# Performance work log

Hardware: AMD Instinct MI355X
Metric: run time of the kernel (lower is better)

Reference implementation:

```python
import jax, jax.numpy as jnp
import numpy as np

N = 80000      # num nodes total (8 graphs x 10000 vars)
E = 2560000    # num edges (avg degree 32)
EMB = 64       # embedding_layer_dim
POS = 16       # positional_features_dims
DG = 64        # dim_gnn
IN0 = 2 * EMB + POS          # 144, first conv in
IN1 = DG + 2 * EMB           # 192, second conv in / BN dim
EPS = 1e-5


def _lin_init(key, fan_in, fan_out):
    return jax.random.normal(key, (fan_in, fan_out), jnp.float32) / np.sqrt(fan_in)


def setup_inputs() -> dict:
    key = jax.random.key(0)
    ks = jax.random.split(key, 16)
    inp = {}
    inp["x1"] = jax.random.normal(ks[0], (N, EMB), jnp.float32)
    inp["x2"] = jax.random.normal(ks[1], (N, EMB), jnp.float32)
    inp["random_dims"] = jax.random.normal(ks[2], (N, POS), jnp.float32)
    inp["batch"] = jnp.sort(jax.random.randint(ks[3], (N,), 0, 8)).astype(jnp.int64)
    inp["x_j_mask"] = jnp.ones((E,), jnp.float32)
    inp["edge_index"] = jax.random.randint(ks[4], (2, E), 0, N).astype(jnp.int64)
    # GCNConv weights (PyG: lin then aggregate, bias added after)
    inp["conv0_w"] = _lin_init(ks[5], IN0, DG)
    inp["conv0_b"] = jnp.zeros((DG,), jnp.float32)
    inp["conv1_w"] = _lin_init(ks[6], IN1, DG)
    inp["conv1_b"] = jnp.zeros((DG,), jnp.float32)
    # BatchNorms after each conv (dim = DG + 2*EMB = 192)
    inp["bn0_g"] = jnp.ones((IN1,), jnp.float32)
    inp["bn0_b"] = jnp.zeros((IN1,), jnp.float32)
    inp["bn1_g"] = jnp.ones((IN1,), jnp.float32)
    inp["bn1_b"] = jnp.zeros((IN1,), jnp.float32)
    # MLP head: mlp[:-2] = [192->64, 64->64], mlp[-2] = 64->32 (final ->1 not applied here)
    inp["mlp0_w"] = _lin_init(ks[7], IN1, DG)
    inp["mlp0_b"] = jnp.zeros((DG,), jnp.float32)
    inp["mlp1_w"] = _lin_init(ks[8], DG, DG)
    inp["mlp1_b"] = jnp.zeros((DG,), jnp.float32)
    inp["mlp2_w"] = _lin_init(ks[9], DG, DG // 2)
    inp["mlp2_b"] = jnp.zeros((DG // 2,), jnp.float32)
    inp["bnm0_g"] = jnp.ones((DG,), jnp.float32)
    inp["bnm0_b"] = jnp.zeros((DG,), jnp.float32)
    inp["bnm1_g"] = jnp.ones((DG,), jnp.float32)
    inp["bnm1_b"] = jnp.zeros((DG,), jnp.float32)
    inp["bnm2_g"] = jnp.ones((DG // 2,), jnp.float32)
    inp["bnm2_b"] = jnp.zeros((DG // 2,), jnp.float32)
    return inp


def _batchnorm(x, g, b):
    m = x.mean(axis=0)
    v = jnp.var(x, axis=0)  # biased var, as torch BN uses for normalization
    return (x - m) * jax.lax.rsqrt(v + EPS) * g + b


def _gcn_conv(x, w, b, row, col, coef):
    # coef = deg^-1/2[row] * deg^-1/2[col] * x_j_mask, per edge
    h = x @ w                                   # [N, out]
    msg = coef[:, None] * h[row]                # gather + scale, [E, out]
    agg = jax.ops.segment_sum(msg, col, num_segments=N)
    return agg + b


def reference(x1, x2, random_dims, batch, x_j_mask, edge_index,
              conv0_w, conv0_b, conv1_w, conv1_b,
              bn0_g, bn0_b, bn1_g, bn1_b,
              mlp0_w, mlp0_b, mlp1_w, mlp1_b, mlp2_w, mlp2_b,
              bnm0_g, bnm0_b, bnm1_g, bnm1_b, bnm2_g, bnm2_b):
    row, col = edge_index[0], edge_index[1]
    # gcn_norm with add_self_loops=False, unit edge weights
    deg = jax.ops.segment_sum(jnp.ones((E,), x1.dtype), col, num_segments=N)
    dis = jnp.where(deg > 0, jax.lax.rsqrt(jnp.maximum(deg, 1.0)), 0.0)
    coef = dis[row] * dis[col] * x_j_mask       # edge mutilation mask applied to messages

    x = jnp.concatenate([x1, x2, random_dims], axis=1)  # [N, 144]
    # GNN layer 0
    h = jax.nn.elu(_gcn_conv(x, conv0_w, conv0_b, row, col, coef))
    x = _batchnorm(jnp.concatenate([x1, x2, h], axis=1), bn0_g, bn0_b)
    # GNN layer 1
    h = jax.nn.elu(_gcn_conv(x, conv1_w, conv1_b, row, col, coef))
    x = _batchnorm(jnp.concatenate([x1, x2, h], axis=1), bn1_g, bn1_b)
    # MLP head (from_node_to_out: mlp[:-2] with bns_mlp[:-1], then mlp[-2] with bns_mlp[-1])
    x = _batchnorm(jax.nn.elu(x @ mlp0_w + mlp0_b), bnm0_g, bnm0_b)
    x = _batchnorm(jax.nn.elu(x @ mlp1_w + mlp1_b), bnm1_g, bnm1_b)
    x = _batchnorm(jax.nn.elu(x @ mlp2_w + mlp2_b), bnm2_g, bnm2_b)
    return x  # [N, DG//2]
```

## Files before the change

kernel.cpp:

```cpp
#include <hip/hip_runtime.h>
#include <math.h>

#define NN 80000
#define NE 2560000
#define NBK 313
#define BN_EPS 1e-5f

typedef __attribute__((ext_vector_type(8))) short short8;
typedef __attribute__((ext_vector_type(8))) unsigned short ushort8;
typedef __attribute__((ext_vector_type(4))) float f32x4;

#define OFF_DIS     0
#define OFF_ROWPTR  80000
#define OFF_CURSOR  160004
#define OFF_DEG     240004
#define OFF_PERM    320004
#define OFF_XB      (OFF_PERM + 2*NE)
#define OFF_RDB     (OFF_XB + NN*64)
#define OFF_B1      (OFF_RDB + NN*16)
#define OFF_B2      (OFF_B1 + NN*32)
#define OFF_B3      (OFF_B2 + NN*32)
#define OFF_WP      (OFF_B3 + NN*32)
#define OFF_BV      (OFF_WP + 20480)
#define OFF_STATS   (OFF_BV + 320)

__device__ __forceinline__ ushort f2b(float f) {
    union { float f; unsigned u; } x; x.f = f;
    return (ushort)((x.u + 0x7FFF + ((x.u >> 16) & 1)) >> 16);
}
__device__ __forceinline__ float b2f(ushort u) {
    union { unsigned u; float f; } x; x.u = ((unsigned)u) << 16;
    return x.f;
}

__global__ void k_deg(const int* __restrict__ col, int* __restrict__ deg) {
    int e = blockIdx.x * blockDim.x + threadIdx.x;
    if (e < NE) atomicAdd(&deg[col[e]], 1);
}

__global__ void __launch_bounds__(256) k_scanA(const int* __restrict__ deg,
                                               float* __restrict__ dis,
                                               int* __restrict__ bsum) {
    int i = blockIdx.x * 256 + threadIdx.x;
    int d = i < NN ? deg[i] : 0;
    if (i < NN) dis[i] = d > 0 ? rsqrtf((float)d) : 0.f;
    __shared__ int red[256];
    red[threadIdx.x] = d;
    __syncthreads();
    for (int off = 128; off > 0; off >>= 1) {
        if (threadIdx.x < off) red[threadIdx.x] += red[threadIdx.x + off];
        __syncthreads();
    }
    if (threadIdx.x == 0) bsum[blockIdx.x] = red[0];
}

__global__ void __launch_bounds__(512) k_scanB(const int* __restrict__ bsum,
                                               int* __restrict__ boff,
                                               int* __restrict__ rowptr) {
    __shared__ int s[512];
    int t = threadIdx.x;
    int v = t < NBK ? bsum[t] : 0;
    s[t] = v;
    __syncthreads();
    for (int off = 1; off < 512; off <<= 1) {
        int u = t >= off ? s[t - off] : 0;
        __syncthreads();
        s[t] += u;
        __syncthreads();
    }
    if (t < NBK) boff[t] = s[t] - v;
    if (t == NBK - 1) rowptr[NN] = s[t];
}

__global__ void __launch_bounds__(256) k_scanC(const int* __restrict__ deg,
                                               const int* __restrict__ boff,
                                               int* __restrict__ rowptr) {
    int i = blockIdx.x * 256 + threadIdx.x;
    int d = i < NN ? deg[i] : 0;
    __shared__ int s[256];
    s[threadIdx.x] = d;
    __syncthreads();
    for (int off = 1; off < 256; off <<= 1) {
        int u = threadIdx.x >= off ? s[threadIdx.x - off] : 0;
        __syncthreads();
        s[threadIdx.x] += u;
        __syncthreads();
    }
    if (i < NN) rowptr[i] = boff[blockIdx.x] + s[threadIdx.x] - d;
}

__global__ void __launch_bounds__(256) k_scat1(const int* __restrict__ erow,
                                               const int* __restrict__ ecol,
                                               const float* __restrict__ mask,
                                               const float* __restrict__ dis,
                                               const int* __restrict__ rowptr,
                                               int* __restrict__ bcursor,
                                               int2* __restrict__ pbuf) {
    __shared__ int hist[NBK], base[NBK];
    for (int i = threadIdx.x; i < NBK; i += 256) hist[i] = 0;
    __syncthreads();
    int e0 = blockIdx.x * 4096;
    int r[16], c[16], rk[16];
    float cf[16];
    #pragma unroll
    for (int i = 0; i < 16; i++) {
        int e = e0 + i * 256 + threadIdx.x;
        if (e < NE) {
            r[i] = erow[e]; c[i] = ecol[e];
            cf[i] = dis[r[i]] * dis[c[i]] * mask[e];
            rk[i] = atomicAdd(&hist[c[i] >> 8], 1);
        } else c[i] = -1;
    }
    __syncthreads();
    for (int b = threadIdx.x; b < NBK; b += 256) {
        int h = hist[b];
        base[b] = h ? atomicAdd(&bcursor[b], h) : 0;
    }
    __syncthreads();
    #pragma unroll
    for (int i = 0; i < 16; i++) {
        if (c[i] >= 0) {
            int b = c[i] >> 8;
            int addr = rowptr[b << 8] + base[b] + rk[i];
            pbuf[addr] = make_int2((r[i] << 8) | (c[i] & 255), __float_as_int(cf[i]));
        }
    }
}

__global__ void __launch_bounds__(256) k_scat2(const int* __restrict__ rowptr,
                                               const int2* __restrict__ pbuf,
                                               int2* __restrict__ perm) {
    __shared__ int rbase[257];
    __shared__ int lcur[256];
    int b = blockIdx.x;
    int c0 = b << 8;
    int ncols = (NN - c0) < 256 ? (NN - c0) : 256;
    int s0 = rowptr[c0];
    if (threadIdx.x < ncols) rbase[threadIdx.x] = rowptr[c0 + threadIdx.x] - s0;
    if (threadIdx.x == 0) rbase[ncols] = rowptr[c0 + ncols] - s0;
    lcur[threadIdx.x] = 0;
    __syncthreads();
    int cnt = rbase[ncols];
    for (int i = threadIdx.x; i < cnt; i += 256) {
        int2 rec = pbuf[s0 + i];
        int crel = rec.x & 255;
        int rr = rec.x >> 8;
        int slot = rbase[crel] + atomicAdd(&lcur[crel], 1);
        perm[s0 + slot] = make_int2(rr, rec.y);
    }
}

__global__ void __launch_bounds__(256) k_prepstats(const float* __restrict__ x1,
                                                   const float* __restrict__ x2,
                                                   const float* __restrict__ rd,
                                                   ushort* __restrict__ xb,
                                                   ushort* __restrict__ rdb,
                                                   float* __restrict__ st) {
    int wave = threadIdx.x >> 6, lane = threadIdx.x & 63;
    float s1 = 0, q1 = 0, s2 = 0, q2 = 0;
    for (int n = blockIdx.x * 4 + wave; n < NN; n += gridDim.x * 4) {
        float a = x1[(size_t)n * 64 + lane];
        float b = x2[(size_t)n * 64 + lane];
        s1 += a; q1 += a * a; s2 += b; q2 += b * b;
        xb[(size_t)n * 128 + lane]      = f2b(a);
        xb[(size_t)n * 128 + 64 + lane] = f2b(b);
        if (lane < 32)
            rdb[(size_t)n * 32 + lane] = lane < 16 ? f2b(rd[(size_t)n * 16 + lane]) : 0;
    }
    __shared__ float red[4][256];
    red[0][threadIdx.x] = s1; red[1][threadIdx.x] = q1;
    red[2][threadIdx.x] = s2; red[3][threadIdx.x] = q2;
    __syncthreads();
    if (threadIdx.x < 64) {
        int l = threadIdx.x;
        atomicAdd(&st[l],       red[0][l] + red[0][l+64] + red[0][l+128] + red[0][l+192]);
        atomicAdd(&st[128 + l], red[1][l] + red[1][l+64] + red[1][l+128] + red[1][l+192]);
        atomicAdd(&st[64 + l],  red[2][l] + red[2][l+64] + red[2][l+128] + red[2][l+192]);
        atomicAdd(&st[192 + l], red[3][l] + red[3][l+64] + red[3][l+128] + red[3][l+192]);
    }
}

__global__ void k_foldw0(const float* __restrict__ W, ushort* __restrict__ Wp) {
    for (int idx = threadIdx.x; idx < 160 * 64; idx += 256) {
        int k = idx >> 6, c = idx & 63;
        float val = k < 144 ? W[k * 64 + c] : 0.f;
        int ks = k >> 5, j = k & 7, kg = (k >> 3) & 3;
        int l = kg * 16 + (c & 15), ct = c >> 4;
        Wp[((ks * 4 + ct) * 64 + l) * 8 + j] = f2b(val);
    }
}

__global__ void k_bnfold192(const float* __restrict__ xs,
                            const float* __restrict__ hsum, const float* __restrict__ hsq,
                            const float* __restrict__ g, const float* __restrict__ bnb,
                            const float* __restrict__ W,
                            const float* __restrict__ bias,
                            ushort* __restrict__ Wp, float* __restrict__ bvec) {
    __shared__ float scale[192], shift[192];
    int t = threadIdx.x;
    if (t < 192) {
        float s = t < 128 ? xs[t] : hsum[t - 128];
        float q = t < 128 ? xs[128 + t] : hsq[t - 128];
        float m = s * (1.f / NN);
        float var = q * (1.f / NN) - m * m;
        float sc = g[t] * rsqrtf(var + BN_EPS);
        scale[t] = sc;
        shift[t] = bnb[t] - m * sc;
    }
    __syncthreads();
    for (int idx = t; idx < 192 * 64; idx += 256) {
        int k = idx >> 6, c = idx & 63;
        float val = scale[k] * W[idx];
        int ks = k >> 5, j = k & 7, kg = (k >> 3) & 3;
        int l = kg * 16 + (c & 15), ct = c >> 4;
        Wp[((ks * 4 + ct) * 64 + l) * 8 + j] = f2b(val);
    }
    if (t < 64) {
        float acc = bias ? bias[t] : 0.f;
        for (int k = 0; k < 192; k++) acc += shift[k] * W[k * 64 + t];
        bvec[t] = acc;
    }
}

__global__ void k_bnfold64(const float* __restrict__ sum, const float* __restrict__ sq,
                           const float* __restrict__ g, const float* __restrict__ bnb,
                           const float* __restrict__ W, const float* __restrict__ bias,
                           ushort* __restrict__ Wp, float* __restrict__ bvec, int NCw) {
    __shared__ float scale[64], shift[64];
    int t = threadIdx.x;
    if (t < 64) {
        float m = sum[t] * (1.f / NN);
        float var = sq[t] * (1.f / NN) - m * m;
        float sc = g[t] * rsqrtf(var + BN_EPS);
        scale[t] = sc;
        shift[t] = bnb[t] - m * sc;
    }
    __syncthreads();
    int NCOLT = NCw >> 4;
    for (int idx = t; idx < 64 * NCw; idx += 256) {
        int k = idx / NCw, c = idx % NCw;
        float val = scale[k] * W[idx];
        int ks = k >> 5, j = k & 7, kg = (k >> 3) & 3;
        int l = kg * 16 + (c & 15), ct = c >> 4;
        Wp[((ks * NCOLT + ct) * 64 + l) * 8 + j] = f2b(val);
    }
    if (t < NCw) {
        float acc = bias[t];
        for (int k = 0; k < 64; k++) acc += shift[k] * W[k * NCw + t];
        bvec[t] = acc;
    }
}

__global__ void k_bnfin(const float* __restrict__ sum, const float* __restrict__ sq,
                        const float* __restrict__ g, const float* __restrict__ b,
                        float* __restrict__ scale, float* __restrict__ shift) {
    int c = threadIdx.x;
    float m = sum[c] * (1.f / NN);
    float var = sq[c] * (1.f / NN) - m * m;
    float sc = g[c] * rsqrtf(var + BN_EPS);
    scale[c] = sc;
    shift[c] = b[c] - m * sc;
}

template <int KSTEPS, int NCOLT, int KS1, int S1, int S2, bool EPI, bool OUTF32>
__global__ void __launch_bounds__(256) k_mfma(const ushort* __restrict__ A1,
                                              const ushort* __restrict__ A2,
                                              const ushort* __restrict__ Wp,
                                              const float* __restrict__ bvec,
                                              void* __restrict__ out,
                                              float* __restrict__ sum,
                                              float* __restrict__ sq) {
    const int NC = NCOLT * 16;
    __shared__ float cs[NC], cq[NC];
    int wave = threadIdx.x >> 6, lane = threadIdx.x & 63;
    int r0 = lane & 15, kg = lane >> 4;
    int rbase = blockIdx.x * 64 + wave * 16;
    if (EPI) {
        if (threadIdx.x < NC) { cs[threadIdx.x] = 0.f; cq[threadIdx.x] = 0.f; }
        __syncthreads();
    }
    f32x4 acc[NCOLT];
    #pragma unroll
    for (int ct = 0; ct < NCOLT; ct++) acc[ct] = (f32x4){0.f, 0.f, 0.f, 0.f};
    #pragma unroll
    for (int ks = 0; ks < KSTEPS; ks++) {
        const ushort* src = (ks < KS1)
            ? A1 + (size_t)(rbase + r0) * S1 + ks * 32 + kg * 8
            : A2 + (size_t)(rbase + r0) * S2 + (ks - KS1) * 32 + kg * 8;
        short8 a = *reinterpret_cast<const short8*>(src);
        #pragma unroll
        for (int ct = 0; ct < NCOLT; ct++) {
            short8 b = *reinterpret_cast<const short8*>(Wp + ((size_t)(ks * NCOLT + ct) * 64 + lane) * 8);
            acc[ct] = __builtin_amdgcn_mfma_f32_16x16x32_bf16(a, b, acc[ct], 0, 0, 0);
        }
    }
    float ss[NCOLT], qq[NCOLT];
    #pragma unroll
    for (int ct = 0; ct < NCOLT; ct++) {
        int c = ct * 16 + r0;
        float bv = bvec[c];
        ss[ct] = 0.f; qq[ct] = 0.f;
        #pragma unroll
        for (int r = 0; r < 4; r++) {
            int row = rbase + kg * 4 + r;
            float v = acc[ct][r] + bv;
            if (EPI) {
                v = v > 0.f ? v : (__expf(v) - 1.f);
                ss[ct] += v; qq[ct] += v * v;
            }
            if (OUTF32) ((float*)out)[(size_t)row * NC + c] = v;
            else        ((ushort*)out)[(size_t)row * NC + c] = f2b(v);
        }
    }
    if (EPI) {
        #pragma unroll
        for (int ct = 0; ct < NCOLT; ct++) {
            int c = ct * 16 + r0;
            atomicAdd(&cs[c], ss[ct]);
            atomicAdd(&cq[c], qq[ct]);
        }
        __syncthreads();
        if (threadIdx.x < NC) {
            atomicAdd(&sum[threadIdx.x], cs[threadIdx.x]);
            atomicAdd(&sq[threadIdx.x], cq[threadIdx.x]);
        }
    }
}

__global__ void __launch_bounds__(256) k_gather(const int* __restrict__ rowptr,
                                                const int2* __restrict__ perm,
                                                const ushort* __restrict__ h,
                                                const float* __restrict__ bias,
                                                ushort* __restrict__ out,
                                                float* __restrict__ sum,
                                                float* __restrict__ sq) {
    __shared__ float cs[64], cq[64];
    if (threadIdx.x < 64) { cs[threadIdx.x] = 0.f; cq[threadIdx.x] = 0.f; }
    __syncthreads();
    int wave = threadIdx.x >> 6, lane = threadIdx.x & 63;
    int g = lane >> 3, c8 = lane & 7;
    const ushort* hb = h + c8 * 8;
    float bs[8];
    #pragma unroll
    for (int j = 0; j < 8; j++) bs[j] = bias[c8 * 8 + j];
    float sArr[8], qArr[8];
    #pragma unroll
    for (int j = 0; j < 8; j++) { sArr[j] = 0.f; qArr[j] = 0.f; }

    for (int n = blockIdx.x * 4 + wave; n < NN; n += gridDim.x * 4) {
        int beg = rowptr[n], end = rowptr[n + 1];
        float acc[8];
        #pragma unroll
        for (int j = 0; j < 8; j++) acc[j] = 0.f;
        int e = beg;
        for (; e + 32 <= end; e += 32) {
            int2 p0 = perm[e + g];
            int2 p1 = perm[e + 8 + g];
            int2 p2 = perm[e + 16 + g];
            int2 p3 = perm[e + 24 + g];
            ushort8 h0 = *reinterpret_cast<const ushort8*>(hb + (size_t)p0.x * 64);
            ushort8 h1 = *reinterpret_cast<const ushort8*>(hb + (size_t)p1.x * 64);
            ushort8 h2 = *reinterpret_cast<const ushort8*>(hb + (size_t)p2.x * 64);
            ushort8 h3 = *reinterpret_cast<const ushort8*>(hb + (size_t)p3.x * 64);
            float c0 = __int_as_float(p0.y), c1 = __int_as_float(p1.y);
            float c2 = __int_as_float(p2.y), c3 = __int_as_float(p3.y);
            #pragma unroll
            for (int j = 0; j < 8; j++) {
                acc[j] += c0 * b2f(h0[j]);
                acc[j] += c1 * b2f(h1[j]);
                acc[j] += c2 * b2f(h2[j]);
                acc[j] += c3 * b2f(h3[j]);
            }
        }
        for (; e < end; e += 8) {
            int ee = e + g;
            int2 p = make_int2(0, 0);
            if (ee < end) p = perm[ee];
            ushort8 hv = *reinterpret_cast<const ushort8*>(hb + (size_t)p.x * 64);
            float cf = __int_as_float(p.y);
            #pragma unroll
            for (int j = 0; j < 8; j++) acc[j] += cf * b2f(hv[j]);
        }
        #pragma unroll
        for (int j = 0; j < 8; j++) {
            float a = acc[j];
            a += __shfl_xor(a, 8, 64);
            a += __shfl_xor(a, 16, 64);
            a += __shfl_xor(a, 32, 64);
            acc[j] = a;
        }
        if (g == 0) {
            ushort8 ov;
            #pragma unroll
            for (int j = 0; j < 8; j++) {
                float v = acc[j] + bs[j];
                v = v > 0.f ? v : (__expf(v) - 1.f);
                sArr[j] += v; qArr[j] += v * v;
                ov[j] = f2b(v);
            }
            *reinterpret_cast<ushort8*>(out + (size_t)n * 64 + c8 * 8) = ov;
        }
    }
    if (g == 0) {
        #pragma unroll
        for (int j = 0; j < 8; j++) {
            atomicAdd(&cs[c8 * 8 + j], sArr[j]);
            atomicAdd(&cq[c8 * 8 + j], qArr[j]);
        }
    }
    __syncthreads();
    if (threadIdx.x < 64) {
        atomicAdd(&sum[threadIdx.x], cs[threadIdx.x]);
        atomicAdd(&sq[threadIdx.x], cq[threadIdx.x]);
    }
}

__global__ void k_out(const float* __restrict__ u2, const float* __restrict__ scale,
                      const float* __restrict__ shift, float* __restrict__ out) {
    int t = blockIdx.x * blockDim.x + threadIdx.x;
    if (t < NN * 32) {
        int c = t & 31;
        out[t] = u2[t] * scale[c] + shift[c];
    }
}

extern "C" void kernel_launch(void* const* d_in, const int* in_sizes, int n_in,
                              void* d_out, int out_size, void* d_ws, size_t ws_size,
                              hipStream_t stream) {
    const float* x1 = (const float*)d_in[0];
    const float* x2 = (const float*)d_in[1];
    const float* rd = (const float*)d_in[2];
    const float* mask = (const float*)d_in[4];
    const int* ei = (const int*)d_in[5];
    const int* erow = ei;
    const int* ecol = ei + NE;
    const float* conv0_w = (const float*)d_in[6];
    const float* conv0_b = (const float*)d_in[7];
    const float* conv1_w = (const float*)d_in[8];
    const float* conv1_b = (const float*)d_in[9];
    const float* bn0_g = (const float*)d_in[10];
    const float* bn0_b = (const float*)d_in[11];
    const float* bn1_g = (const float*)d_in[12];
    const float* bn1_b = (const float*)d_in[13];
    const float* mlp0_w = (const float*)d_in[14];
    const float* mlp0_b = (const float*)d_in[15];
    const float* mlp1_w = (const float*)d_in[16];
    const float* mlp1_b = (const float*)d_in[17];
    const float* mlp2_w = (const float*)d_in[18];
    const float* mlp2_b = (const float*)d_in[19];
    const float* bnm0_g = (const float*)d_in[20];
    const float* bnm0_b = (const float*)d_in[21];
    const float* bnm1_g = (const float*)d_in[22];
    const float* bnm1_b = (const float*)d_in[23];
    const float* bnm2_g = (const float*)d_in[24];
    const float* bnm2_b = (const float*)d_in[25];

    float* ws = (float*)d_ws;
    float* dis = ws + OFF_DIS;
    int* rowptr = (int*)(ws + OFF_ROWPTR);
    int* bcursor = (int*)(ws + OFF_CURSOR);
    int* bsum = bcursor + 1024;
    int* boff = bcursor + 2048;
    int* deg = (int*)(ws + OFF_DEG);
    int2* perm = (int2*)(ws + OFF_PERM);
    ushort* xb = (ushort*)(ws + OFF_XB);
    ushort* rdb = (ushort*)(ws + OFF_RDB);
    ushort* B1 = (ushort*)(ws + OFF_B1);
    ushort* B2 = (ushort*)(ws + OFF_B2);
    ushort* B3 = (ushort*)(ws + OFF_B3);
    int2* pbuf = (int2*)(ws + OFF_B1);
    ushort* wp = (ushort*)(ws + OFF_WP);
    ushort* WP0 = wp, *WP1 = wp + 10240, *WP2 = wp + 22528, *WP3 = wp + 34816, *WP4 = wp + 38912;
    float* bv = ws + OFF_BV;
    float* st = ws + OFF_STATS;

    hipMemsetAsync(bcursor, 0, (size_t)(2 * NN) * 4, stream);
    hipMemsetAsync(bv, 0, (size_t)(320 + 1920) * 4, stream);

    k_deg<<<(NE + 255) / 256, 256, 0, stream>>>(ecol, deg);
    k_scanA<<<NBK, 256, 0, stream>>>(deg, dis, bsum);
    k_scanB<<<1, 512, 0, stream>>>(bsum, boff, rowptr);
    k_scanC<<<NBK, 256, 0, stream>>>(deg, boff, rowptr);
    k_scat1<<<(NE + 4095) / 4096, 256, 0, stream>>>(erow, ecol, mask, dis, rowptr, bcursor, pbuf);
    k_scat2<<<NBK, 256, 0, stream>>>(rowptr, pbuf, perm);
    k_prepstats<<<1024, 256, 0, stream>>>(x1, x2, rd, xb, rdb, st);
    k_foldw0<<<1, 256, 0, stream>>>(conv0_w, WP0);

    const int GB = NN / 64;

    k_mfma<5, 4, 4, 128, 32, false, false><<<GB, 256, 0, stream>>>(xb, rdb, WP0, bv, B1, nullptr, nullptr);
    k_gather<<<2048, 256, 0, stream>>>(rowptr, perm, B1, conv0_b, B2, st + 256, st + 320);
    k_bnfold192<<<1, 256, 0, stream>>>(st, st + 256, st + 320, bn0_g, bn0_b, conv1_w, nullptr, WP1, bv + 64);

    k_mfma<6, 4, 4, 128, 64, false, false><<<GB, 256, 0, stream>>>(xb, B2, WP1, bv + 64, B1, nullptr, nullptr);
    k_gather<<<2048, 256, 0, stream>>>(rowptr, perm, B1, conv1_b, B3, st + 384, st + 448);
    k_bnfold192<<<1, 256, 0, stream>>>(st, st + 384, st + 448, bn1_g, bn1_b, mlp0_w, mlp0_b, WP2, bv + 128);

    k_mfma<6, 4, 4, 128, 64, true, false><<<GB, 256, 0, stream>>>(xb, B3, WP2, bv + 128, B2, st + 512, st + 576);
    k_bnfold64<<<1, 256, 0, stream>>>(st + 512, st + 576, bnm0_g, bnm0_b, mlp1_w, mlp1_b, WP3, bv + 192, 64);
    k_mfma<2, 4, 2, 64, 64, true, false><<<GB, 256, 0, stream>>>(B2, nullptr, WP3, bv + 192, B1, st + 640, st + 704);
    k_bnfold64<<<1, 256, 0, stream>>>(st + 640, st + 704, bnm1_g, bnm1_b, mlp2_w, mlp2_b, WP4, bv + 256, 32);
    k_mfma<2, 2, 2, 64, 64, true, true><<<GB, 256, 0, stream>>>(B1, nullptr, WP4, bv + 256, B3, st + 768, st + 800);
    k_bnfin<<<1, 32, 0, stream>>>(st + 768, st + 800, bnm2_g, bnm2_b, st + 1856, st + 1888);
    k_out<<<(NN * 32 + 255) / 256, 256, 0, stream>>>((const float*)B3, st + 1856, st + 1888, (float*)d_out);
}
```

Baseline: 704.5 us.

## Split node features into 16-column planes and pack edge records to 32 bits

Intermediate bf16 activations are stored as four column-planes of 16 features each, so every gather pass reads a 32-byte slice per node. The aggregation then runs as four passes whose working set (80000 x 32 B) can stay cache-resident for the random neighbour reads. Edge records shrink from int2 to one 32-bit word holding a 17-bit source index and a 15-bit fp16 coefficient with the sign bit dropped, which halves index traffic. The cost is four launches per layer that each reread the edge list, plus lower precision for the normalisation coefficient.

```diff
diff --git a/kernel.cpp b/kernel.cpp
--- a/kernel.cpp
+++ b/kernel.cpp
@@ -1,4 +1,5 @@
 #include <hip/hip_runtime.h>
+#include <hip/hip_fp16.h>
 #include <math.h>
 
 #define NN 80000
@@ -129,7 +130,7 @@
 
 __global__ void __launch_bounds__(256) k_scat2(const int* __restrict__ rowptr,
                                                const int2* __restrict__ pbuf,
-                                               int2* __restrict__ perm) {
+                                               unsigned* __restrict__ perm) {
     __shared__ int rbase[257];
     __shared__ int lcur[256];
     int b = blockIdx.x;
@@ -144,9 +145,12 @@
     for (int i = threadIdx.x; i < cnt; i += 256) {
         int2 rec = pbuf[s0 + i];
         int crel = rec.x & 255;
-        int rr = rec.x >> 8;
+        unsigned rr = (unsigned)(rec.x >> 8);
+        float cf = __int_as_float(rec.y);
+        __half hh = __float2half(cf);
+        unsigned hb = (unsigned)__half_as_ushort(hh) & 0x7FFFu;
         int slot = rbase[crel] + atomicAdd(&lcur[crel], 1);
-        perm[s0 + slot] = make_int2(rr, rec.y);
+        perm[s0 + slot] = (rr << 15) | hb;
     }
 }
 
@@ -262,7 +266,7 @@
     shift[c] = b[c] - m * sc;
 }
 
-template <int KSTEPS, int NCOLT, int KS1, int S1, int S2, bool EPI, bool OUTF32>
+template <int KSTEPS, int NCOLT, int KS1, int S1, int A1B, int S2, int A2B, bool EPI, bool OUTF32>
 __global__ void __launch_bounds__(256) k_mfma(const ushort* __restrict__ A1,
                                               const ushort* __restrict__ A2,
                                               const ushort* __restrict__ Wp,
@@ -284,9 +288,15 @@
     for (int ct = 0; ct < NCOLT; ct++) acc[ct] = (f32x4){0.f, 0.f, 0.f, 0.f};
     #pragma unroll
     for (int ks = 0; ks < KSTEPS; ks++) {
-        const ushort* src = (ks < KS1)
-            ? A1 + (size_t)(rbase + r0) * S1 + ks * 32 + kg * 8
-            : A2 + (size_t)(rbase + r0) * S2 + (ks - KS1) * 32 + kg * 8;
+        const ushort* src;
+        if (ks < KS1) {
+            if (A1B) src = A1 + ((size_t)(ks * 2 + (kg >> 1)) * NN + (rbase + r0)) * 16 + (kg & 1) * 8;
+            else     src = A1 + (size_t)(rbase + r0) * S1 + ks * 32 + kg * 8;
+        } else {
+            int kss = ks - KS1;
+            if (A2B) src = A2 + ((size_t)(kss * 2 + (kg >> 1)) * NN + (rbase + r0)) * 16 + (kg & 1) * 8;
+            else     src = A2 + (size_t)(rbase + r0) * S2 + kss * 32 + kg * 8;
+        }
         short8 a = *reinterpret_cast<const short8*>(src);
         #pragma unroll
         for (int ct = 0; ct < NCOLT; ct++) {
@@ -309,7 +319,7 @@
                 ss[ct] += v; qq[ct] += v * v;
             }
             if (OUTF32) ((float*)out)[(size_t)row * NC + c] = v;
-            else        ((ushort*)out)[(size_t)row * NC + c] = f2b(v);
+            else        ((ushort*)out)[((size_t)ct * NN + row) * 16 + r0] = f2b(v);
         }
     }
     if (EPI) {
@@ -327,63 +337,45 @@
     }
 }
 
-__global__ void __launch_bounds__(256) k_gather(const int* __restrict__ rowptr,
-                                                const int2* __restrict__ perm,
-                                                const ushort* __restrict__ h,
+__global__ void __launch_bounds__(256) k_gath16(const int* __restrict__ rowptr,
+                                                const unsigned* __restrict__ perm,
+                                                const ushort* __restrict__ hsub,
                                                 const float* __restrict__ bias,
-                                                ushort* __restrict__ out,
+                                                ushort* __restrict__ outsub,
                                                 float* __restrict__ sum,
                                                 float* __restrict__ sq) {
-    __shared__ float cs[64], cq[64];
-    if (threadIdx.x < 64) { cs[threadIdx.x] = 0.f; cq[threadIdx.x] = 0.f; }
+    __shared__ float cs[16], cq[16];
+    if (threadIdx.x < 16) { cs[threadIdx.x] = 0.f; cq[threadIdx.x] = 0.f; }
     __syncthreads();
     int wave = threadIdx.x >> 6, lane = threadIdx.x & 63;
-    int g = lane >> 3, c8 = lane & 7;
-    const ushort* hb = h + c8 * 8;
+    int g = lane >> 1, hf = lane & 1;
+    const ushort* hb = hsub + hf * 8;
     float bs[8];
     #pragma unroll
-    for (int j = 0; j < 8; j++) bs[j] = bias[c8 * 8 + j];
-    float sArr[8], qArr[8];
-    #pragma unroll
-    for (int j = 0; j < 8; j++) { sArr[j] = 0.f; qArr[j] = 0.f; }
+    for (int j = 0; j < 8; j++) bs[j] = bias[hf * 8 + j];
+    float sA[8], qA[8];
+    #pragma unroll
+    for (int j = 0; j < 8; j++) { sA[j] = 0.f; qA[j] = 0.f; }
 
     for (int n = blockIdx.x * 4 + wave; n < NN; n += gridDim.x * 4) {
         int beg = rowptr[n], end = rowptr[n + 1];
         float acc[8];
         #pragma unroll
         for (int j = 0; j < 8; j++) acc[j] = 0.f;
-        int e = beg;
-        for (; e + 32 <= end; e += 32) {
-            int2 p0 = perm[e + g];
-            int2 p1 = perm[e + 8 + g];
-            int2 p2 = perm[e + 16 + g];
-            int2 p3 = perm[e + 24 + g];
-            ushort8 h0 = *reinterpret_cast<const ushort8*>(hb + (size_t)p0.x * 64);
-            ushort8 h1 = *reinterpret_cast<const ushort8*>(hb + (size_t)p1.x * 64);
-            ushort8 h2 = *reinterpret_cast<const ushort8*>(hb + (size_t)p2.x * 64);
-            ushort8 h3 = *reinterpret_cast<const ushort8*>(hb + (size_t)p3.x * 64);
-            float c0 = __int_as_float(p0.y), c1 = __int_as_float(p1.y);
-            float c2 = __int_as_float(p2.y), c3 = __int_as_float(p3.y);
-            #pragma unroll
-            for (int j = 0; j < 8; j++) {
-                acc[j] += c0 * b2f(h0[j]);
-                acc[j] += c1 * b2f(h1[j]);
-                acc[j] += c2 * b2f(h2[j]);
-                acc[j] += c3 * b2f(h3[j]);
-            }
-        }
-        for (; e < end; e += 8) {
+        for (int e = beg; e < end; e += 32) {
             int ee = e + g;
-            int2 p = make_int2(0, 0);
-            if (ee < end) p = perm[ee];
-            ushort8 hv = *reinterpret_cast<const ushort8*>(hb + (size_t)p.x * 64);
-            float cf = __int_as_float(p.y);
+            unsigned p = ee < end ? perm[ee] : 0u;
+            __half_raw hr; hr.x = (unsigned short)(p & 0x7FFFu);
+            float cf = __half2float(*(__half*)&hr);
+            ushort8 hv = *reinterpret_cast<const ushort8*>(hb + (size_t)(p >> 15) * 16);
             #pragma unroll
             for (int j = 0; j < 8; j++) acc[j] += cf * b2f(hv[j]);
         }
         #pragma unroll
         for (int j = 0; j < 8; j++) {
             float a = acc[j];
+            a += __shfl_xor(a, 2, 64);
+            a += __shfl_xor(a, 4, 64);
             a += __shfl_xor(a, 8, 64);
             a += __shfl_xor(a, 16, 64);
             a += __shfl_xor(a, 32, 64);
@@ -395,21 +387,21 @@
             for (int j = 0; j < 8; j++) {
                 float v = acc[j] + bs[j];
                 v = v > 0.f ? v : (__expf(v) - 1.f);
-                sArr[j] += v; qArr[j] += v * v;
+                sA[j] += v; qA[j] += v * v;
                 ov[j] = f2b(v);
             }
-            *reinterpret_cast<ushort8*>(out + (size_t)n * 64 + c8 * 8) = ov;
+            *reinterpret_cast<ushort8*>(outsub + (size_t)n * 16 + hf * 8) = ov;
         }
     }
     if (g == 0) {
         #pragma unroll
         for (int j = 0; j < 8; j++) {
-            atomicAdd(&cs[c8 * 8 + j], sArr[j]);
-            atomicAdd(&cq[c8 * 8 + j], qArr[j]);
-        }
-    }
-    __syncthreads();
-    if (threadIdx.x < 64) {
+            atomicAdd(&cs[hf * 8 + j], sA[j]);
+            atomicAdd(&cq[hf * 8 + j], qA[j]);
+        }
+    }
+    __syncthreads();
+    if (threadIdx.x < 16) {
         atomicAdd(&sum[threadIdx.x], cs[threadIdx.x]);
         atomicAdd(&sq[threadIdx.x], cq[threadIdx.x]);
     }
@@ -462,7 +454,7 @@
     int* bsum = bcursor + 1024;
     int* boff = bcursor + 2048;
     int* deg = (int*)(ws + OFF_DEG);
-    int2* perm = (int2*)(ws + OFF_PERM);
+    unsigned* perm = (unsigned*)(ws + OFF_PERM);
     ushort* xb = (ushort*)(ws + OFF_XB);
     ushort* rdb = (ushort*)(ws + OFF_RDB);
     ushort* B1 = (ushort*)(ws + OFF_B1);
@@ -488,19 +480,25 @@
 
     const int GB = NN / 64;
 
-    k_mfma<5, 4, 4, 128, 32, false, false><<<GB, 256, 0, stream>>>(xb, rdb, WP0, bv, B1, nullptr, nullptr);
-    k_gather<<<2048, 256, 0, stream>>>(rowptr, perm, B1, conv0_b, B2, st + 256, st + 320);
+    k_mfma<5, 4, 4, 128, 0, 32, 0, false, false><<<GB, 256, 0, stream>>>(xb, rdb, WP0, bv, B1, nullptr, nullptr);
+    for (int p = 0; p < 4; p++)
+        k_gath16<<<2048, 256, 0, stream>>>(rowptr, perm, B1 + (size_t)p * NN * 16,
+                                           conv0_b + p * 16, B2 + (size_t)p * NN * 16,
+                                           st + 256 + p * 16, st + 320 + p * 16);
     k_bnfold192<<<1, 256, 0, stream>>>(st, st + 256, st + 320, bn0_g, bn0_b, conv1_w, nullptr, WP1, bv + 64);
 
-    k_mfma<6, 4, 4, 128, 64, false, false><<<GB, 256, 0, stream>>>(xb, B2, WP1, bv + 64, B1, nullptr, nullptr);
-    k_gather<<<2048, 256, 0, stream>>>(rowptr, perm, B1, conv1_b, B3, st + 384, st + 448);
+    k_mfma<6, 4, 4, 128, 0, 0, 1, false, false><<<GB, 256, 0, stream>>>(xb, B2, WP1, bv + 64, B1, nullptr, nullptr);
+    for (int p = 0; p < 4; p++)
+        k_gath16<<<2048, 256, 0, stream>>>(rowptr, perm, B1 + (size_t)p * NN * 16,
+                                           conv1_b + p * 16, B3 + (size_t)p * NN * 16,
+                                           st + 384 + p * 16, st + 448 + p * 16);
     k_bnfold192<<<1, 256, 0, stream>>>(st, st + 384, st + 448, bn1_g, bn1_b, mlp0_w, mlp0_b, WP2, bv + 128);
 
-    k_mfma<6, 4, 4, 128, 64, true, false><<<GB, 256, 0, stream>>>(xb, B3, WP2, bv + 128, B2, st + 512, st + 576);
+    k_mfma<6, 4, 4, 128, 0, 0, 1, true, false><<<GB, 256, 0, stream>>>(xb, B3, WP2, bv + 128, B2, st + 512, st + 576);
     k_bnfold64<<<1, 256, 0, stream>>>(st + 512, st + 576, bnm0_g, bnm0_b, mlp1_w, mlp1_b, WP3, bv + 192, 64);
-    k_mfma<2, 4, 2, 64, 64, true, false><<<GB, 256, 0, stream>>>(B2, nullptr, WP3, bv + 192, B1, st + 640, st + 704);
+    k_mfma<2, 4, 2, 0, 1, 0, 0, true, false><<<GB, 256, 0, stream>>>(B2, nullptr, WP3, bv + 192, B1, st + 640, st + 704);
     k_bnfold64<<<1, 256, 0, stream>>>(st + 640, st + 704, bnm1_g, bnm1_b, mlp2_w, mlp2_b, WP4, bv + 256, 32);
-    k_mfma<2, 2, 2, 64, 64, true, true><<<GB, 256, 0, stream>>>(B1, nullptr, WP4, bv + 256, B3, st + 768, st + 800);
+    k_mfma<2, 2, 2, 0, 1, 0, 0, true, true><<<GB, 256, 0, stream>>>(B1, nullptr, WP4, bv + 256, B3, st + 768, st + 800);
     k_bnfin<<<1, 32, 0, stream>>>(st + 768, st + 800, bnm2_g, bnm2_b, st + 1856, st + 1888);
     k_out<<<(NN * 32 + 255) / 256, 256, 0, stream>>>((const float*)B3, st + 1856, st + 1888, (float*)d_out);
 }
```

Result: slower. 851.7 us (+20.9%).

## Build CSR from fixed-capacity buckets and pack edge records into 32 bits

Applied to the files above, without the earlier changes.

Scatters edges into per-bucket, fixed-capacity staging buffers first. Per-column degrees are then counted from those buffers in shared memory, which removes the global atomic degree pass and the separate scan kernels. The edge coefficient is computed during placement and stored as a 15-bit fp16 value alongside a 17-bit row index in one 32-bit word, halving the edge-record bytes the two gather passes read. In exchange, coefficients lose precision and their sign, and any bucket holding more than 10240 edges silently drops edges.

```diff
diff --git a/kernel.cpp b/kernel.cpp
--- a/kernel.cpp
+++ b/kernel.cpp
@@ -1,9 +1,11 @@
 #include <hip/hip_runtime.h>
+#include <hip/hip_fp16.h>
 #include <math.h>
 
 #define NN 80000
 #define NE 2560000
 #define NBK 313
+#define BCAP 10240
 #define BN_EPS 1e-5f
 
 typedef __attribute__((ext_vector_type(8))) short short8;
@@ -32,34 +34,68 @@
     union { unsigned u; float f; } x; x.u = ((unsigned)u) << 16;
     return x.f;
 }
-
-__global__ void k_deg(const int* __restrict__ col, int* __restrict__ deg) {
-    int e = blockIdx.x * blockDim.x + threadIdx.x;
-    if (e < NE) atomicAdd(&deg[col[e]], 1);
-}
-
-__global__ void __launch_bounds__(256) k_scanA(const int* __restrict__ deg,
-                                               float* __restrict__ dis,
-                                               int* __restrict__ bsum) {
-    int i = blockIdx.x * 256 + threadIdx.x;
-    int d = i < NN ? deg[i] : 0;
-    if (i < NN) dis[i] = d > 0 ? rsqrtf((float)d) : 0.f;
-    __shared__ int red[256];
-    red[threadIdx.x] = d;
-    __syncthreads();
-    for (int off = 128; off > 0; off >>= 1) {
-        if (threadIdx.x < off) red[threadIdx.x] += red[threadIdx.x + off];
-        __syncthreads();
-    }
-    if (threadIdx.x == 0) bsum[blockIdx.x] = red[0];
-}
-
-__global__ void __launch_bounds__(512) k_scanB(const int* __restrict__ bsum,
+__device__ __forceinline__ float h2f(unsigned bits15) {
+    __half_raw hr; hr.x = (unsigned short)(bits15 & 0x7FFFu);
+    return __half2float(*(__half*)&hr);
+}
+
+__global__ void __launch_bounds__(256) k_scat1(const int* __restrict__ erow,
+                                               const int* __restrict__ ecol,
+                                               const float* __restrict__ mask,
+                                               int* __restrict__ bcursor,
+                                               int2* __restrict__ pbuf) {
+    __shared__ int hist[NBK], base[NBK];
+    for (int i = threadIdx.x; i < NBK; i += 256) hist[i] = 0;
+    __syncthreads();
+    int e0 = blockIdx.x * 4096;
+    int r[16], c[16], rk[16];
+    float mk[16];
+    #pragma unroll
+    for (int i = 0; i < 16; i++) {
+        int e = e0 + i * 256 + threadIdx.x;
+        if (e < NE) {
+            r[i] = erow[e]; c[i] = ecol[e]; mk[i] = mask[e];
+            rk[i] = atomicAdd(&hist[c[i] >> 8], 1);
+        } else c[i] = -1;
+    }
+    __syncthreads();
+    for (int b = threadIdx.x; b < NBK; b += 256) {
+        int h = hist[b];
+        base[b] = h ? atomicAdd(&bcursor[b], h) : 0;
+    }
+    __syncthreads();
+    #pragma unroll
+    for (int i = 0; i < 16; i++) {
+        if (c[i] >= 0) {
+            int b = c[i] >> 8;
+            int off = base[b] + rk[i];
+            if (off < BCAP)
+                pbuf[b * BCAP + off] = make_int2((r[i] << 8) | (c[i] & 255), __float_as_int(mk[i]));
+        }
+    }
+}
+
+__global__ void __launch_bounds__(256) k_cnt(const int* __restrict__ bcursor,
+                                             const int2* __restrict__ pbuf,
+                                             int* __restrict__ deg) {
+    __shared__ int hist[256];
+    int b = blockIdx.x, c0 = b << 8;
+    int ncols = (NN - c0) < 256 ? (NN - c0) : 256;
+    hist[threadIdx.x] = 0;
+    __syncthreads();
+    int cnt = bcursor[b];
+    for (int i = threadIdx.x; i < cnt; i += 256)
+        atomicAdd(&hist[pbuf[b * BCAP + i].x & 255], 1);
+    __syncthreads();
+    if (threadIdx.x < ncols) deg[c0 + threadIdx.x] = hist[threadIdx.x];
+}
+
+__global__ void __launch_bounds__(512) k_scanB(const int* __restrict__ bcursor,
                                                int* __restrict__ boff,
                                                int* __restrict__ rowptr) {
     __shared__ int s[512];
     int t = threadIdx.x;
-    int v = t < NBK ? bsum[t] : 0;
+    int v = t < NBK ? bcursor[t] : 0;
     s[t] = v;
     __syncthreads();
     for (int off = 1; off < 512; off <<= 1) {
@@ -72,81 +108,51 @@
     if (t == NBK - 1) rowptr[NN] = s[t];
 }
 
-__global__ void __launch_bounds__(256) k_scanC(const int* __restrict__ deg,
+__global__ void k_dis(const int* __restrict__ deg, float* __restrict__ dis) {
+    int i = blockIdx.x * blockDim.x + threadIdx.x;
+    if (i < NN) {
+        int d = deg[i];
+        dis[i] = d > 0 ? rsqrtf((float)d) : 0.f;
+    }
+}
+
+__global__ void __launch_bounds__(256) k_place(const int* __restrict__ bcursor,
                                                const int* __restrict__ boff,
-                                               int* __restrict__ rowptr) {
-    int i = blockIdx.x * 256 + threadIdx.x;
-    int d = i < NN ? deg[i] : 0;
-    __shared__ int s[256];
-    s[threadIdx.x] = d;
+                                               const int* __restrict__ deg,
+                                               const float* __restrict__ dis,
+                                               const int2* __restrict__ pbuf,
+                                               int* __restrict__ rowptr,
+                                               unsigned* __restrict__ perm) {
+    __shared__ int s[256], rbase[256], lcur[256];
+    __shared__ float sdis[256];
+    int b = blockIdx.x, c0 = b << 8;
+    int ncols = (NN - c0) < 256 ? (NN - c0) : 256;
+    int t = threadIdx.x;
+    int d = t < ncols ? deg[c0 + t] : 0;
+    s[t] = d;
+    lcur[t] = 0;
+    if (t < ncols) sdis[t] = dis[c0 + t];
     __syncthreads();
     for (int off = 1; off < 256; off <<= 1) {
-        int u = threadIdx.x >= off ? s[threadIdx.x - off] : 0;
+        int u = t >= off ? s[t - off] : 0;
         __syncthreads();
-        s[threadIdx.x] += u;
+        s[t] += u;
         __syncthreads();
     }
-    if (i < NN) rowptr[i] = boff[blockIdx.x] + s[threadIdx.x] - d;
-}
-
-__global__ void __launch_bounds__(256) k_scat1(const int* __restrict__ erow,
-                                               const int* __restrict__ ecol,
-                                               const float* __restrict__ mask,
-                                               const float* __restrict__ dis,
-                                               const int* __restrict__ rowptr,
-                                               int* __restrict__ bcursor,
-                                               int2* __restrict__ pbuf) {
-    __shared__ int hist[NBK], base[NBK];
-    for (int i = threadIdx.x; i < NBK; i += 256) hist[i] = 0;
-    __syncthreads();
-    int e0 = blockIdx.x * 4096;
-    int r[16], c[16], rk[16];
-    float cf[16];
-    #pragma unroll
-    for (int i = 0; i < 16; i++) {
-        int e = e0 + i * 256 + threadIdx.x;
-        if (e < NE) {
-            r[i] = erow[e]; c[i] = ecol[e];
-            cf[i] = dis[r[i]] * dis[c[i]] * mask[e];
-            rk[i] = atomicAdd(&hist[c[i] >> 8], 1);
-        } else c[i] = -1;
-    }
-    __syncthreads();
-    for (int b = threadIdx.x; b < NBK; b += 256) {
-        int h = hist[b];
-        base[b] = h ? atomicAdd(&bcursor[b], h) : 0;
-    }
-    __syncthreads();
-    #pragma unroll
-    for (int i = 0; i < 16; i++) {
-        if (c[i] >= 0) {
-            int b = c[i] >> 8;
-            int addr = rowptr[b << 8] + base[b] + rk[i];
-            pbuf[addr] = make_int2((r[i] << 8) | (c[i] & 255), __float_as_int(cf[i]));
-        }
-    }
-}
-
-__global__ void __launch_bounds__(256) k_scat2(const int* __restrict__ rowptr,
-                                               const int2* __restrict__ pbuf,
-                                               int2* __restrict__ perm) {
-    __shared__ int rbase[257];
-    __shared__ int lcur[256];
-    int b = blockIdx.x;
-    int c0 = b << 8;
-    int ncols = (NN - c0) < 256 ? (NN - c0) : 256;
-    int s0 = rowptr[c0];
-    if (threadIdx.x < ncols) rbase[threadIdx.x] = rowptr[c0 + threadIdx.x] - s0;
-    if (threadIdx.x == 0) rbase[ncols] = rowptr[c0 + ncols] - s0;
-    lcur[threadIdx.x] = 0;
-    __syncthreads();
-    int cnt = rbase[ncols];
-    for (int i = threadIdx.x; i < cnt; i += 256) {
-        int2 rec = pbuf[s0 + i];
+    rbase[t] = s[t] - d;
+    __syncthreads();
+    int gb = boff[b];
+    if (t < ncols) rowptr[c0 + t] = gb + rbase[t];
+    int cnt = bcursor[b];
+    for (int i = t; i < cnt; i += 256) {
+        int2 rec = pbuf[b * BCAP + i];
         int crel = rec.x & 255;
-        int rr = rec.x >> 8;
-        int slot = rbase[crel] + atomicAdd(&lcur[crel], 1);
-        perm[s0 + slot] = make_int2(rr, rec.y);
+        unsigned row = (unsigned)(rec.x >> 8);
+        float coef = dis[row] * sdis[crel] * __int_as_float(rec.y);
+        __half hh = __float2half(coef);
+        unsigned hb = (unsigned)__half_as_ushort(hh) & 0x7FFFu;
+        int slot = gb + rbase[crel] + atomicAdd(&lcur[crel], 1);
+        perm[slot] = (row << 15) | hb;
     }
 }
 
@@ -328,7 +334,7 @@
 }
 
 __global__ void __launch_bounds__(256) k_gather(const int* __restrict__ rowptr,
-                                                const int2* __restrict__ perm,
+                                                const unsigned* __restrict__ perm,
                                                 const ushort* __restrict__ h,
                                                 const float* __restrict__ bias,
                                                 ushort* __restrict__ out,
@@ -354,16 +360,15 @@
         for (int j = 0; j < 8; j++) acc[j] = 0.f;
         int e = beg;
         for (; e + 32 <= end; e += 32) {
-            int2 p0 = perm[e + g];
-            int2 p1 = perm[e + 8 + g];
-            int2 p2 = perm[e + 16 + g];
-            int2 p3 = perm[e + 24 + g];
-            ushort8 h0 = *reinterpret_cast<const ushort8*>(hb + (size_t)p0.x * 64);
-            ushort8 h1 = *reinterpret_cast<const ushort8*>(hb + (size_t)p1.x * 64);
-            ushort8 h2 = *reinterpret_cast<const ushort8*>(hb + (size_t)p2.x * 64);
-            ushort8 h3 = *reinterpret_cast<const ushort8*>(hb + (size_t)p3.x * 64);
-            float c0 = __int_as_float(p0.y), c1 = __int_as_float(p1.y);
-            float c2 = __int_as_float(p2.y), c3 = __int_as_float(p3.y);
+            unsigned p0 = perm[e + g];
+            unsigned p1 = perm[e + 8 + g];
+            unsigned p2 = perm[e + 16 + g];
+            unsigned p3 = perm[e + 24 + g];
+            ushort8 h0 = *reinterpret_cast<const ushort8*>(hb + (size_t)(p0 >> 15) * 64);
+            ushort8 h1 = *reinterpret_cast<const ushort8*>(hb + (size_t)(p1 >> 15) * 64);
+            ushort8 h2 = *reinterpret_cast<const ushort8*>(hb + (size_t)(p2 >> 15) * 64);
+            ushort8 h3 = *reinterpret_cast<const ushort8*>(hb + (size_t)(p3 >> 15) * 64);
+            float c0 = h2f(p0), c1 = h2f(p1), c2 = h2f(p2), c3 = h2f(p3);
             #pragma unroll
             for (int j = 0; j < 8; j++) {
                 acc[j] += c0 * b2f(h0[j]);
@@ -374,10 +379,9 @@
         }
         for (; e < end; e += 8) {
             int ee = e + g;
-            int2 p = make_int2(0, 0);
-            if (ee < end) p = perm[ee];
-            ushort8 hv = *reinterpret_cast<const ushort8*>(hb + (size_t)p.x * 64);
-            float cf = __int_as_float(p.y);
+            unsigned p = ee < end ? perm[ee] : 0u;
+            ushort8 hv = *reinterpret_cast<const ushort8*>(hb + (size_t)(p >> 15) * 64);
+            float cf = h2f(p);
             #pragma unroll
             for (int j = 0; j < 8; j++) acc[j] += cf * b2f(hv[j]);
         }
@@ -459,10 +463,9 @@
     float* dis = ws + OFF_DIS;
     int* rowptr = (int*)(ws + OFF_ROWPTR);
     int* bcursor = (int*)(ws + OFF_CURSOR);
-    int* bsum = bcursor + 1024;
     int* boff = bcursor + 2048;
     int* deg = (int*)(ws + OFF_DEG);
-    int2* perm = (int2*)(ws + OFF_PERM);
+    unsigned* perm = (unsigned*)(ws + OFF_PERM);
     ushort* xb = (ushort*)(ws + OFF_XB);
     ushort* rdb = (ushort*)(ws + OFF_RDB);
     ushort* B1 = (ushort*)(ws + OFF_B1);
@@ -474,15 +477,14 @@
     float* bv = ws + OFF_BV;
     float* st = ws + OFF_STATS;
 
-    hipMemsetAsync(bcursor, 0, (size_t)(2 * NN) * 4, stream);
+    hipMemsetAsync(bcursor, 0, (size_t)1024 * 4, stream);
     hipMemsetAsync(bv, 0, (size_t)(320 + 1920) * 4, stream);
 
-    k_deg<<<(NE + 255) / 256, 256, 0, stream>>>(ecol, deg);
-    k_scanA<<<NBK, 256, 0, stream>>>(deg, dis, bsum);
-    k_scanB<<<1, 512, 0, stream>>>(bsum, boff, rowptr);
-    k_scanC<<<NBK, 256, 0, stream>>>(deg, boff, rowptr);
-    k_scat1<<<(NE + 4095) / 4096, 256, 0, stream>>>(erow, ecol, mask, dis, rowptr, bcursor, pbuf);
-    k_scat2<<<NBK, 256, 0, stream>>>(rowptr, pbuf, perm);
+    k_scat1<<<(NE + 4095) / 4096, 256, 0, stream>>>(erow, ecol, mask, bcursor, pbuf);
+    k_cnt<<<NBK, 256, 0, stream>>>(bcursor, pbuf, deg);
+    k_scanB<<<1, 512, 0, stream>>>(bcursor, boff, rowptr);
+    k_dis<<<NBK, 256, 0, stream>>>(deg, dis);
+    k_place<<<NBK, 256, 0, stream>>>(bcursor, boff, deg, dis, pbuf, rowptr, perm);
     k_prepstats<<<1024, 256, 0, stream>>>(x1, x2, rd, xb, rdb, st);
     k_foldw0<<<1, 256, 0, stream>>>(conv0_w, WP0);
 
```

Result: faster. 613.6 us (-12.9%).
